# Performance work log

Hardware: AMD Instinct MI355X
Metric: run time of the kernel (lower is better)

The kernel has to match this reference:

```python
import jax, jax.numpy as jnp
import numpy as np

N = 50000
E = 1600000
F_IN = 256
HEADS = 4
HID = 32
C = 16
NEG_SLOPE = 0.2


def _add_self_loops(edge_index, n):
    loop = jnp.arange(n, dtype=edge_index.dtype)
    return jnp.concatenate([edge_index, jnp.stack([loop, loop])], axis=1)


def gat_conv(x, edge_index, W, att_src, att_dst, bias, heads, n):
    # PyG GATConv (concat=True, add_self_loops=True, inference: no dropout)
    ei = _add_self_loops(edge_index, n)
    src, dst = ei[0], ei[1]
    d = W.shape[1] // heads
    xw = (x @ W).reshape(n, heads, d)                      # [N,H,D]
    a_src = jnp.sum(xw * att_src, axis=-1)                 # [N,H]
    a_dst = jnp.sum(xw * att_dst, axis=-1)                 # [N,H]
    e = jax.nn.leaky_relu(a_src[src] + a_dst[dst], NEG_SLOPE)  # [E',H]
    # segment softmax over destination neighborhoods
    m = jax.ops.segment_max(e, dst, num_segments=n)        # [N,H]
    ex = jnp.exp(e - m[dst])
    denom = jax.ops.segment_sum(ex, dst, num_segments=n)   # [N,H]
    alpha = ex / denom[dst]                                # [E',H]
    msg = xw[src] * alpha[:, :, None]                      # [E',H,D]
    out = jax.ops.segment_sum(msg, dst, num_segments=n)    # [N,H,D]
    return out.reshape(n, heads * d) + bias


def setup_inputs() -> dict:
    key = jax.random.key(0)
    ks = jax.random.split(key, 10)
    g = lambda k, shape, fan: jax.random.normal(k, shape, jnp.float32) * (1.0 / np.sqrt(fan))
    x = jax.random.normal(ks[0], (N, F_IN), jnp.float32)
    edge_index = jax.random.randint(ks[1], (2, E), 0, N, dtype=jnp.int64)
    return {
        "x": x,
        "edge_index": edge_index,
        "W1": g(ks[2], (F_IN, HEADS * HID), F_IN),
        "att_src1": g(ks[3], (HEADS, HID), HID),
        "att_dst1": g(ks[4], (HEADS, HID), HID),
        "b1": jnp.zeros((HEADS * HID,), jnp.float32),
        "W2": g(ks[5], (HEADS * HID, C), HEADS * HID),
        "att_src2": g(ks[6], (1, C), C),
        "att_dst2": g(ks[7], (1, C), C),
        "b2": jnp.zeros((C,), jnp.float32),
    }


def reference(x, edge_index, W1, att_src1, att_dst1, b1, W2, att_src2, att_dst2, b2):
    h = gat_conv(x, edge_index, W1, att_src1, att_dst1, b1, HEADS, N)
    h = jax.nn.relu(h)
    # dropout: identity at inference (training=False)
    out = gat_conv(h, edge_index, W2, att_src2, att_dst2, b2, 1, N)
    return jax.nn.log_softmax(out, axis=1)
```

## Files before the change

### kernel.cpp

```cpp
#include <hip/hip_runtime.h>
#include <hip/hip_bf16.h>

typedef __hip_bfloat16 bf16;
typedef long long i64;
typedef unsigned long long u64;
typedef __attribute__((ext_vector_type(8))) short short8;
typedef __attribute__((ext_vector_type(4))) float floatx4;

#define NN    50000
#define EE    1600000
#define E2    1650000
#define FIN   256
#define HD    128
#define NH    4
#define NC    16
#define SLOPE 0.2f
#define K     128
#define DPB   391
#define CAPB  16384
#define CAP   15360
#define CH2   2048

#define KS_S  2312

#define OF_FLAGS 0
#define OF_BCUR  16
#define OF_BBASE 144
#define OF_RP    280
#define OF_W1T   50284
#define OF_BIN   66668
#define OF_CSR   4260972
#define OF_XQ    5910972
#define OF_SC    7510972
#define OF_AS1   7610972
#define OF_AD1   7810972
#define OF_HW2   8010972
#define OF_AS2   8810972
#define OF_AD2   8860972

__device__ __forceinline__ float b2f(bf16 v) { return __bfloat162float(v); }
__device__ __forceinline__ float us2f(unsigned short u) {
    return __uint_as_float(((unsigned)u) << 16);
}
__device__ __forceinline__ unsigned short f2us(float f) {
    unsigned u = __float_as_uint(f);
    return (unsigned short)((u + 0x7fffu + ((u >> 16) & 1u)) >> 16);
}
__device__ __forceinline__ float lrelu(float v) { return v > 0.f ? v : SLOPE * v; }
__device__ __forceinline__ float sb2f(unsigned u, int sh) {
    return (float)((int)(u << (24 - sh)) >> 24);
}
__device__ __forceinline__ int fwi(int node, int ch) {
    return node * 132 + (ch >> 5) * 33 + (ch & 31);
}

template <bool F32>
__device__ __forceinline__ float ldin(const void* p, int i) {
    if (F32) return ((const float*)p)[i];
    return b2f(((const bf16*)p)[i]);
}
template <bool F32>
__device__ __forceinline__ float4 ldin4(const void* p, int i) {
    if (F32) return *(const float4*)((const float*)p + i);
    ushort4 u = *(const ushort4*)((const unsigned short*)p + i);
    float4 r;
    r.x = us2f(u.x); r.y = us2f(u.y); r.z = us2f(u.z); r.w = us2f(u.w);
    return r;
}

__device__ __forceinline__ void edge_sd(const void* ei, int f64, int e, int& s, int& d) {
    if (e >= EE) { s = e - EE; d = s; return; }
    if (f64) {
        s = (int)((const i64*)ei)[e];
        d = (int)((const i64*)ei)[EE + e];
    } else {
        s = ((const int*)ei)[e];
        d = ((const int*)ei)[EE + e];
    }
    s = min(max(s, 0), NN - 1);
    d = min(max(d, 0), NN - 1);
}

__global__ void detect(const void* x, const void* ei, int* flags, int* bcur) {
    __shared__ int cnt[2];
    int t = threadIdx.x;
    if (t < K) bcur[t] = t * CAPB;
    if (t == 0) { cnt[0] = 0; cnt[1] = 0; }
    __syncthreads();
    const unsigned short* xb = (const unsigned short*)x;
    int c0 = 0;
    for (int i = t; i < 4096; i += 256) {
        float v = __uint_as_float(((unsigned)xb[2 * i]) << 16);
        if (!(fabsf(v) < 1e6f)) c0++;
    }
    const i64* e64 = (const i64*)ei;
    int c1 = 0;
    for (int i = t; i < 1024; i += 256) {
        i64 v = e64[i];
        if (v >= 0 && v < NN) c1++;
    }
    atomicAdd(&cnt[0], c0);
    atomicAdd(&cnt[1], c1);
    __syncthreads();
    if (t == 0) {
        flags[0] = (cnt[0] > 400) ? 1 : 0;
        flags[1] = (cnt[1] >= 1000) ? 1 : 0;
    }
}

template <bool F32>
__global__ void trW(const void* __restrict__ W1, const int* __restrict__ flags,
                    unsigned short* __restrict__ w1t) {
    if (flags[0] != (F32 ? 1 : 0)) return;
    int t = blockIdx.x * 256 + threadIdx.x;
    int k = t >> 5, n4 = (t & 31) * 4;
    float4 v = ldin4<F32>(W1, k * HD + n4);
    int ks = k >> 5, kk = k & 31;
    w1t[((ks * HD + n4 + 0) * 32) + kk] = f2us(v.x);
    w1t[((ks * HD + n4 + 1) * 32) + kk] = f2us(v.y);
    w1t[((ks * HD + n4 + 2) * 32) + kk] = f2us(v.z);
    w1t[((ks * HD + n4 + 3) * 32) + kk] = f2us(v.w);
}

__global__ __launch_bounds__(256) void binScatter(const void* __restrict__ ei,
                                                  const int* __restrict__ flags,
                                                  int* __restrict__ bcur,
                                                  u64* __restrict__ bin) {
    __shared__ int h[K], res[K];
    int t = threadIdx.x;
    int base = blockIdx.x * CH2 + t * 8;
    if (t < K) h[t] = 0;
    __syncthreads();
    int f64 = flags[1];
    int sv[8], dv[8], rk[8];
    int n_ = 0;
    if (!f64 && base + 8 <= EE) {
        const int* es = (const int*)ei;
        int4 a = *(const int4*)&es[base];
        int4 b = *(const int4*)&es[base + 4];
        int4 c = *(const int4*)&es[EE + base];
        int4 g = *(const int4*)&es[EE + base + 4];
        sv[0] = a.x; sv[1] = a.y; sv[2] = a.z; sv[3] = a.w;
        sv[4] = b.x; sv[5] = b.y; sv[6] = b.z; sv[7] = b.w;
        dv[0] = c.x; dv[1] = c.y; dv[2] = c.z; dv[3] = c.w;
        dv[4] = g.x; dv[5] = g.y; dv[6] = g.z; dv[7] = g.w;
#pragma unroll
        for (int i = 0; i < 8; i++) {
            sv[i] = min(max(sv[i], 0), NN - 1);
            dv[i] = min(max(dv[i], 0), NN - 1);
        }
        n_ = 8;
    } else {
        for (int i = 0; i < 8; i++) {
            int e = base + i;
            if (e < E2) {
                int s, d; edge_sd(ei, f64, e, s, d);
                sv[n_] = s; dv[n_] = d; n_++;
            }
        }
    }
#pragma unroll 8
    for (int i = 0; i < n_; i++) rk[i] = atomicAdd(&h[dv[i] / DPB], 1);
    __syncthreads();
    if (t < K) res[t] = h[t] ? atomicAdd(&bcur[t], h[t]) : 0;
    __syncthreads();
#pragma unroll 8
    for (int i = 0; i < n_; i++) {
        int b = dv[i] / DPB;
        int pos = res[b] + rk[i];
        pos = min(pos, (b + 1) * CAPB - 1);
        bin[pos] = (((u64)(unsigned)dv[i]) << 32) | (unsigned)sv[i];
    }
}

__global__ void bucketScan(const int* __restrict__ bcur, int* __restrict__ bbase) {
    __shared__ int sh[K];
    int t = threadIdx.x;
    int v = min(bcur[t] - t * CAPB, CAPB);
    sh[t] = v;
    __syncthreads();
    for (int off = 1; off < K; off <<= 1) {
        int u = (t >= off) ? sh[t - off] : 0;
        __syncthreads();
        sh[t] += u;
        __syncthreads();
    }
    bbase[t] = sh[t] - v;
    if (t == K - 1) bbase[K] = sh[K - 1];
}

__global__ __launch_bounds__(256) void csrB(const u64* __restrict__ bin,
                                            const int* __restrict__ bbase,
                                            int* __restrict__ rp, int* __restrict__ csr) {
    __shared__ int cnt[512];
    __shared__ int cur[DPB];
    __shared__ int buf[CAP];
    int b = blockIdx.x, t = threadIdx.x;
    int d0 = b * DPB;
    int nd = min(DPB, NN - d0);
    int src0 = b * CAPB;
    int base = bbase[b], size = bbase[b + 1] - base;
    cnt[t] = 0; cnt[t + 256] = 0;
    __syncthreads();
    for (int i = t; i < size; i += 256) {
        int d = (int)(bin[src0 + i] >> 32);
        atomicAdd(&cnt[d - d0], 1);
    }
    __syncthreads();
    int a0 = cnt[2 * t], a1 = cnt[2 * t + 1];
    int ps = a0 + a1;
    buf[t] = ps;
    __syncthreads();
    for (int off = 1; off < 256; off <<= 1) {
        int u = (t >= off) ? buf[t - off] : 0;
        __syncthreads();
        buf[t] += u;
        __syncthreads();
    }
    int ex = buf[t] - ps;
    __syncthreads();
    cnt[2 * t] = ex;
    cnt[2 * t + 1] = ex + a0;
    __syncthreads();
    for (int i = t; i < nd; i += 256) {
        rp[d0 + i] = base + cnt[i];
        cur[i] = cnt[i];
    }
    if (b == K - 1 && t == 0) rp[NN] = bbase[K];
    __syncthreads();
    if (size <= CAP) {
        for (int i = t; i < size; i += 256) {
            u64 p = bin[src0 + i];
            int pos = atomicAdd(&cur[(int)(p >> 32) - d0], 1);
            buf[pos] = (int)(unsigned)p;
        }
        __syncthreads();
        for (int i = t; i < size; i += 256) csr[base + i] = buf[i];
    } else {
        for (int i = t; i < size; i += 256) {
            u64 p = bin[src0 + i];
            int pos = base + atomicAdd(&cur[(int)(p >> 32) - d0], 1);
            csr[pos] = (int)(unsigned)p;
        }
    }
}

template <bool F32>
__global__ __launch_bounds__(256) void gemm1(
    const void* __restrict__ x, const unsigned short* __restrict__ w1t,
    const void* __restrict__ as1, const void* __restrict__ ad1,
    const int* __restrict__ flags, signed char* __restrict__ xq, float* __restrict__ sc2,
    float* __restrict__ asrc, float* __restrict__ adst) {
    if (flags[0] != (F32 ? 1 : 0)) return;
    __shared__ unsigned short af[8 * KS_S];
    __shared__ float scl[128];
    int t = threadIdx.x;
    int m0 = blockIdx.x * 64;
#pragma unroll
    for (int i = 0; i < 16; i++) {
        int slot = i * 256 + t;
        int mi = slot >> 6, k4 = (slot & 63) * 4;
        float4 v = make_float4(0.f, 0.f, 0.f, 0.f);
        if (m0 + mi < NN) v = ldin4<F32>(x, (m0 + mi) * FIN + k4);
        ushort4 o;
        o.x = f2us(v.x); o.y = f2us(v.y); o.z = f2us(v.z); o.w = f2us(v.w);
        *(ushort4*)&af[(k4 >> 5) * KS_S + mi * 36 + (k4 & 31)] = o;
    }
    __syncthreads();
    int w = t >> 6, lane = t & 63;
    int col = lane & 15, q = lane >> 4;
    floatx4 acc[4][2];
#pragma unroll
    for (int mt = 0; mt < 4; mt++)
#pragma unroll
        for (int u = 0; u < 2; u++) { acc[mt][u].x = 0.f; acc[mt][u].y = 0.f; acc[mt][u].z = 0.f; acc[mt][u].w = 0.f; }
#pragma unroll
    for (int ks = 0; ks < 8; ks++) {
        short8 bf0 = *(const short8*)&w1t[(ks * HD + w * 32 + col) * 32 + q * 8];
        short8 bf1 = *(const short8*)&w1t[(ks * HD + w * 32 + 16 + col) * 32 + q * 8];
#pragma unroll
        for (int mt = 0; mt < 4; mt++) {
            short8 afr = *(const short8*)&af[ks * KS_S + (mt * 16 + col) * 36 + q * 8];
            acc[mt][0] = __builtin_amdgcn_mfma_f32_16x16x32_bf16(afr, bf0, acc[mt][0], 0, 0, 0);
            acc[mt][1] = __builtin_amdgcn_mfma_f32_16x16x32_bf16(afr, bf1, acc[mt][1], 0, 0, 0);
        }
    }
    __syncthreads();
    float* fw = (float*)af;
#pragma unroll
    for (int mt = 0; mt < 4; mt++)
#pragma unroll
        for (int u = 0; u < 2; u++)
#pragma unroll
            for (int r = 0; r < 4; r++) {
                int node = mt * 16 + q * 4 + r;
                fw[fwi(node, w * 32 + u * 16 + col)] = acc[mt][u][r];
            }
    __syncthreads();
    int node = t >> 2, part = t & 3;
    {
        float amax = 0.f;
#pragma unroll
        for (int c = 0; c < 32; c++) amax = fmaxf(amax, fabsf(fw[fwi(node, part * 32 + c)]));
        amax = fmaxf(amax, __shfl_xor(amax, 1));
        if ((part & 1) == 0) {
            scl[node * 2 + (part >> 1)] = (amax > 0.f) ? 127.f / amax : 0.f;
            if (m0 + node < NN) sc2[(m0 + node) * 2 + (part >> 1)] = amax * (1.f / 127.f);
        }
    }
    __syncthreads();
    if (m0 + node < NN) {
        float inv = scl[node * 2 + (part >> 1)];
        unsigned dw[8];
#pragma unroll
        for (int g = 0; g < 8; g++) {
            unsigned pk = 0;
#pragma unroll
            for (int j = 0; j < 4; j++) {
                float v = fw[fwi(node, part * 32 + g * 4 + j)];
                int qi = (int)rintf(v * inv);
                qi = min(127, max(-127, qi));
                pk |= ((unsigned)(qi & 255)) << (8 * j);
            }
            dw[g] = pk;
        }
        *(uint4*)&xq[(m0 + node) * HD + part * 32]      = make_uint4(dw[0], dw[1], dw[2], dw[3]);
        *(uint4*)&xq[(m0 + node) * HD + part * 32 + 16] = make_uint4(dw[4], dw[5], dw[6], dw[7]);
        float s = 0.f, dd = 0.f;
#pragma unroll
        for (int c = 0; c < 32; c++) {
            float xv = fw[fwi(node, part * 32 + c)];
            s  += xv * ldin<F32>(as1, part * 32 + c);
            dd += xv * ldin<F32>(ad1, part * 32 + c);
        }
        asrc[(m0 + node) * NH + part] = s;
        adst[(m0 + node) * NH + part] = dd;
    }
}

template <bool F32>
__global__ __launch_bounds__(128) void node1(
    const int* __restrict__ rp, const int* __restrict__ cs,
    const float* __restrict__ asrc, const float* __restrict__ adst,
    const signed char* __restrict__ xq, const float* __restrict__ sc2,
    const void* __restrict__ b1, const void* __restrict__ W2,
    const void* __restrict__ as2, const void* __restrict__ ad2,
    const int* __restrict__ flags, float* __restrict__ hw2,
    float* __restrict__ asrc2, float* __restrict__ adst2) {
    if (flags[0] != (F32 ? 1 : 0)) return;
    int d = blockIdx.x, t = threadIdx.x;
    int beg = rp[d], end = rp[d + 1];
    __shared__ float sw[32][4];
    __shared__ int   ss[32];
    __shared__ float red[2][HD];
    __shared__ float wv[2][4];
    __shared__ float hs[HD];
    __shared__ float l2[32];
    int hw_ = t & 3;
    float adw = adst[d * NH + hw_];
    int cg = t & 15, eo = t >> 4, head = cg >> 2;
    float acc[8];
#pragma unroll
    for (int j = 0; j < 8; j++) acc[j] = 0.f;
    float wacc = 0.f;
    const unsigned* xqu = (const unsigned*)xq;
    for (int chb = beg; chb < end; chb += 32) {
        __syncthreads();
        int ec = chb + (t >> 2);
        float w = 0.f, wsc = 0.f;
        int s = 0;
        if (ec < end) {
            s = cs[ec];
            w = __expf(fminf(lrelu(asrc[s * NH + hw_] + adw), 80.f));
            wsc = w * sc2[s * 2 + (hw_ >> 1)];
        }
        sw[t >> 2][hw_] = wsc;
        if (hw_ == 0) ss[t >> 2] = s;
        wacc += w;
        __syncthreads();
        int m = min(32, end - chb);
        for (int e = eo; e < m; e += 8) {
            float we = sw[e][head];
            int s2 = ss[e];
            uint2 u = *(const uint2*)&xqu[s2 * 32 + cg * 2];
            acc[0] += we * sb2f(u.x, 0);
            acc[1] += we * sb2f(u.x, 8);
            acc[2] += we * sb2f(u.x, 16);
            acc[3] += we * sb2f(u.x, 24);
            acc[4] += we * sb2f(u.y, 0);
            acc[5] += we * sb2f(u.y, 8);
            acc[6] += we * sb2f(u.y, 16);
            acc[7] += we * sb2f(u.y, 24);
        }
    }
    wacc += __shfl_xor(wacc, 4);
    wacc += __shfl_xor(wacc, 8);
    wacc += __shfl_xor(wacc, 16);
    wacc += __shfl_xor(wacc, 32);
    int wid = t >> 6, lane = t & 63;
    if (lane < 4) wv[wid][lane] = wacc;
#pragma unroll
    for (int j = 0; j < 8; j++) {
        acc[j] += __shfl_xor(acc[j], 16);
        acc[j] += __shfl_xor(acc[j], 32);
    }
    if (lane < 16) {
#pragma unroll
        for (int j = 0; j < 8; j++) red[wid][lane * 8 + j] = acc[j];
    }
    __syncthreads();
    float tot = red[0][t] + red[1][t];
    float wt  = wv[0][t >> 5] + wv[1][t >> 5];
    hs[t] = fmaxf(tot / wt + ldin<F32>(b1, t), 0.f);
    __syncthreads();
    int j = t & 15, g = t >> 4;
    float p = 0.f;
#pragma unroll
    for (int k = 0; k < 16; k++) p += hs[g * 16 + k] * ldin<F32>(W2, (g * 16 + k) * NC + j);
    p += __shfl_xor(p, 16, 64);
    p += __shfl_xor(p, 32, 64);
    if ((t & 63) < 16) l2[(t >> 6) * 16 + j] = p;
    __syncthreads();
    if (t < 16) {
        float hw = l2[t] + l2[16 + t];
        hw2[d * NC + t] = hw;
        float a2s = hw * ldin<F32>(as2, t);
        float a2d = hw * ldin<F32>(ad2, t);
#pragma unroll
        for (int off = 8; off; off >>= 1) {
            a2s += __shfl_xor(a2s, off, 16);
            a2d += __shfl_xor(a2d, off, 16);
        }
        if (t == 0) { asrc2[d] = a2s; adst2[d] = a2d; }
    }
}

template <bool F32>
__global__ __launch_bounds__(64) void node2(
    const int* __restrict__ rp, const int* __restrict__ cs,
    const float* __restrict__ asrc2, const float* __restrict__ adst2,
    const float* __restrict__ hw2, const void* __restrict__ b2,
    const int* __restrict__ flags, void* __restrict__ out) {
    if (flags[0] != (F32 ? 1 : 0)) return;
    int d = blockIdx.x, t = threadIdx.x;
    int beg = rp[d], end = rp[d + 1];
    float ad = adst2[d];
    __shared__ float sw2[64];
    __shared__ int   ss2[64];
    int q = t & 3, eo = t >> 2;
    float4 acc = make_float4(0.f, 0.f, 0.f, 0.f);
    float wsum = 0.f;
    for (int chb = beg; chb < end; chb += 64) {
        __syncthreads();
        int ec = chb + t;
        float w = 0.f;
        int s = 0;
        if (ec < end) {
            s = cs[ec];
            w = __expf(fminf(lrelu(asrc2[s] + ad), 80.f));
        }
        sw2[t] = w;
        ss2[t] = s;
        __syncthreads();
        int m = min(64, end - chb);
        for (int e = eo; e < m; e += 16) {
            float we = sw2[e];
            float4 v = *(const float4*)&hw2[ss2[e] * NC + q * 4];
            acc.x += we * v.x; acc.y += we * v.y;
            acc.z += we * v.z; acc.w += we * v.w;
            wsum += we;
        }
    }
#pragma unroll
    for (int off = 4; off < 64; off <<= 1) {
        acc.x += __shfl_xor(acc.x, off);
        acc.y += __shfl_xor(acc.y, off);
        acc.z += __shfl_xor(acc.z, off);
        acc.w += __shfl_xor(acc.w, off);
        wsum  += __shfl_xor(wsum, off);
    }
    float rw = 1.f / wsum;
    float v0 = acc.x * rw + ldin<F32>(b2, q * 4 + 0);
    float v1 = acc.y * rw + ldin<F32>(b2, q * 4 + 1);
    float v2 = acc.z * rw + ldin<F32>(b2, q * 4 + 2);
    float v3 = acc.w * rw + ldin<F32>(b2, q * 4 + 3);
    float mx = fmaxf(fmaxf(v0, v1), fmaxf(v2, v3));
    mx = fmaxf(mx, __shfl_xor(mx, 1));
    mx = fmaxf(mx, __shfl_xor(mx, 2));
    float es = __expf(v0 - mx) + __expf(v1 - mx) + __expf(v2 - mx) + __expf(v3 - mx);
    es += __shfl_xor(es, 1);
    es += __shfl_xor(es, 2);
    float lse = mx + __logf(es);
    if (t < 4) {
        if (F32) {
            *(float4*)&((float*)out)[d * NC + q * 4] =
                make_float4(v0 - lse, v1 - lse, v2 - lse, v3 - lse);
        } else {
            bf16* o = (bf16*)out + d * NC + q * 4;
            o[0] = __float2bfloat16(v0 - lse); o[1] = __float2bfloat16(v1 - lse);
            o[2] = __float2bfloat16(v2 - lse); o[3] = __float2bfloat16(v3 - lse);
        }
    }
}

extern "C" void kernel_launch(void* const* d_in, const int* in_sizes, int n_in,
                              void* d_out, int out_size, void* d_ws, size_t ws_size,
                              hipStream_t stream) {
    const void* x   = d_in[0];
    const void* ei  = d_in[1];
    const void* W1  = d_in[2];
    const void* as1 = d_in[3];
    const void* ad1 = d_in[4];
    const void* b1  = d_in[5];
    const void* W2  = d_in[6];
    const void* as2 = d_in[7];
    const void* ad2 = d_in[8];
    const void* b2v = d_in[9];

    float* ws = (float*)d_ws;
    int* flags = (int*)(ws + OF_FLAGS);
    int* bcur  = (int*)(ws + OF_BCUR);
    int* bbase = (int*)(ws + OF_BBASE);
    int* rp    = (int*)(ws + OF_RP);
    unsigned short* w1t = (unsigned short*)(ws + OF_W1T);
    u64* bin   = (u64*)(ws + OF_BIN);
    int* csr   = (int*)(ws + OF_CSR);
    signed char* xq = (signed char*)(ws + OF_XQ);
    float* sc2   = ws + OF_SC;
    float* asrc1 = ws + OF_AS1;
    float* adst1 = ws + OF_AD1;
    float* hw2   = ws + OF_HW2;
    float* asrc2 = ws + OF_AS2;
    float* adst2 = ws + OF_AD2;

    detect<<<1, 256, 0, stream>>>(x, ei, flags, bcur);
    trW<true><<<32, 256, 0, stream>>>(W1, flags, w1t);
    binScatter<<<(E2 + CH2 - 1) / CH2, 256, 0, stream>>>(ei, flags, bcur, bin);
    bucketScan<<<1, K, 0, stream>>>(bcur, bbase);
    csrB<<<K, 256, 0, stream>>>(bin, bbase, rp, csr);

    const int GB = (NN + 63) / 64;
    gemm1<true><<<GB, 256, 0, stream>>>(x, w1t, as1, ad1, flags, xq, sc2, asrc1, adst1);
    node1<true><<<NN, 128, 0, stream>>>(rp, csr, asrc1, adst1, xq, sc2, b1, W2, as2, ad2,
                                        flags, hw2, asrc2, adst2);
    node2<true><<<NN, 64, 0, stream>>>(rp, csr, asrc2, adst2, hw2, b2v, flags, d_out);
}
```

Before: 291.4 us.

## Widen node1 to 256 threads, offset-encode int8, pack four nodes per node2 block

```diff
diff --git a/kernel.cpp b/kernel.cpp
--- a/kernel.cpp
+++ b/kernel.cpp
@@ -47,8 +47,8 @@
     return (unsigned short)((u + 0x7fffu + ((u >> 16) & 1u)) >> 16);
 }
 __device__ __forceinline__ float lrelu(float v) { return v > 0.f ? v : SLOPE * v; }
-__device__ __forceinline__ float sb2f(unsigned u, int sh) {
-    return (float)((int)(u << (24 - sh)) >> 24);
+__device__ __forceinline__ float ub2f(unsigned u, int sh) {
+    return (float)((u >> sh) & 0xffu);
 }
 __device__ __forceinline__ int fwi(int node, int ch) {
     return node * 132 + (ch >> 5) * 33 + (ch & 31);
@@ -320,7 +320,7 @@
                 float v = fw[fwi(node, part * 32 + g * 4 + j)];
                 int qi = (int)rintf(v * inv);
                 qi = min(127, max(-127, qi));
-                pk |= ((unsigned)(qi & 255)) << (8 * j);
+                pk |= ((unsigned)((qi + 128) & 255)) << (8 * j);
             }
             dw[g] = pk;
         }
@@ -339,7 +339,7 @@
 }
 
 template <bool F32>
-__global__ __launch_bounds__(128) void node1(
+__global__ __launch_bounds__(256) void node1(
     const int* __restrict__ rp, const int* __restrict__ cs,
     const float* __restrict__ asrc, const float* __restrict__ adst,
     const signed char* __restrict__ xq, const float* __restrict__ sc2,
@@ -350,21 +350,21 @@
     if (flags[0] != (F32 ? 1 : 0)) return;
     int d = blockIdx.x, t = threadIdx.x;
     int beg = rp[d], end = rp[d + 1];
-    __shared__ float sw[32][4];
-    __shared__ int   ss[32];
-    __shared__ float red[2][HD];
-    __shared__ float wv[2][4];
+    __shared__ float sw[64][5];
+    __shared__ int   ss[64];
+    __shared__ float red[4][HD];
+    __shared__ float wv[4][4];
     __shared__ float hs[HD];
-    __shared__ float l2[32];
+    __shared__ float l2[4][16];
     int hw_ = t & 3;
     float adw = adst[d * NH + hw_];
     int cg = t & 15, eo = t >> 4, head = cg >> 2;
     float acc[8];
 #pragma unroll
     for (int j = 0; j < 8; j++) acc[j] = 0.f;
-    float wacc = 0.f;
+    float wacc = 0.f, wss = 0.f;
     const unsigned* xqu = (const unsigned*)xq;
-    for (int chb = beg; chb < end; chb += 32) {
+    for (int chb = beg; chb < end; chb += 64) {
         __syncthreads();
         int ec = chb + (t >> 2);
         float w = 0.f, wsc = 0.f;
@@ -378,21 +378,25 @@
         if (hw_ == 0) ss[t >> 2] = s;
         wacc += w;
         __syncthreads();
-        int m = min(32, end - chb);
-        for (int e = eo; e < m; e += 8) {
+#pragma unroll
+        for (int k = 0; k < 4; k++) {
+            int e = eo + k * 16;
             float we = sw[e][head];
             int s2 = ss[e];
             uint2 u = *(const uint2*)&xqu[s2 * 32 + cg * 2];
-            acc[0] += we * sb2f(u.x, 0);
-            acc[1] += we * sb2f(u.x, 8);
-            acc[2] += we * sb2f(u.x, 16);
-            acc[3] += we * sb2f(u.x, 24);
-            acc[4] += we * sb2f(u.y, 0);
-            acc[5] += we * sb2f(u.y, 8);
-            acc[6] += we * sb2f(u.y, 16);
-            acc[7] += we * sb2f(u.y, 24);
-        }
-    }
+            acc[0] += we * ub2f(u.x, 0);
+            acc[1] += we * ub2f(u.x, 8);
+            acc[2] += we * ub2f(u.x, 16);
+            acc[3] += we * ub2f(u.x, 24);
+            acc[4] += we * ub2f(u.y, 0);
+            acc[5] += we * ub2f(u.y, 8);
+            acc[6] += we * ub2f(u.y, 16);
+            acc[7] += we * ub2f(u.y, 24);
+            wss += we;
+        }
+    }
+#pragma unroll
+    for (int j = 0; j < 8; j++) acc[j] -= 128.f * wss;
     wacc += __shfl_xor(wacc, 4);
     wacc += __shfl_xor(wacc, 8);
     wacc += __shfl_xor(wacc, 16);
@@ -409,20 +413,22 @@
         for (int j = 0; j < 8; j++) red[wid][lane * 8 + j] = acc[j];
     }
     __syncthreads();
-    float tot = red[0][t] + red[1][t];
-    float wt  = wv[0][t >> 5] + wv[1][t >> 5];
-    hs[t] = fmaxf(tot / wt + ldin<F32>(b1, t), 0.f);
+    if (t < HD) {
+        float tot = red[0][t] + red[1][t] + red[2][t] + red[3][t];
+        float wt  = wv[0][t >> 5] + wv[1][t >> 5] + wv[2][t >> 5] + wv[3][t >> 5];
+        hs[t] = fmaxf(tot / wt + ldin<F32>(b1, t), 0.f);
+    }
     __syncthreads();
     int j = t & 15, g = t >> 4;
     float p = 0.f;
 #pragma unroll
-    for (int k = 0; k < 16; k++) p += hs[g * 16 + k] * ldin<F32>(W2, (g * 16 + k) * NC + j);
-    p += __shfl_xor(p, 16, 64);
-    p += __shfl_xor(p, 32, 64);
-    if ((t & 63) < 16) l2[(t >> 6) * 16 + j] = p;
+    for (int k = 0; k < 8; k++) p += hs[g * 8 + k] * ldin<F32>(W2, (g * 8 + k) * NC + j);
+    p += __shfl_xor(p, 16);
+    p += __shfl_xor(p, 32);
+    if (lane < 16) l2[wid][j] = p;
     __syncthreads();
     if (t < 16) {
-        float hw = l2[t] + l2[16 + t];
+        float hw = l2[0][t] + l2[1][t] + l2[2][t] + l2[3][t];
         hw2[d * NC + t] = hw;
         float a2s = hw * ldin<F32>(as2, t);
         float a2d = hw * ldin<F32>(ad2, t);
@@ -436,39 +442,44 @@
 }
 
 template <bool F32>
-__global__ __launch_bounds__(64) void node2(
+__global__ __launch_bounds__(256) void node2(
     const int* __restrict__ rp, const int* __restrict__ cs,
     const float* __restrict__ asrc2, const float* __restrict__ adst2,
     const float* __restrict__ hw2, const void* __restrict__ b2,
     const int* __restrict__ flags, void* __restrict__ out) {
     if (flags[0] != (F32 ? 1 : 0)) return;
-    int d = blockIdx.x, t = threadIdx.x;
+    int t = threadIdx.x, wid = t >> 6, lane = t & 63;
+    int d = blockIdx.x * 4 + wid;
+    if (d >= NN) return;
     int beg = rp[d], end = rp[d + 1];
     float ad = adst2[d];
-    __shared__ float sw2[64];
-    __shared__ int   ss2[64];
-    int q = t & 3, eo = t >> 2;
+    int q = lane & 3, eo = lane >> 2;
     float4 acc = make_float4(0.f, 0.f, 0.f, 0.f);
-    float wsum = 0.f;
+    float wtot = 0.f;
     for (int chb = beg; chb < end; chb += 64) {
-        __syncthreads();
-        int ec = chb + t;
+        int ec = chb + lane;
         float w = 0.f;
         int s = 0;
         if (ec < end) {
             s = cs[ec];
             w = __expf(fminf(lrelu(asrc2[s] + ad), 80.f));
         }
-        sw2[t] = w;
-        ss2[t] = s;
-        __syncthreads();
-        int m = min(64, end - chb);
-        for (int e = eo; e < m; e += 16) {
-            float we = sw2[e];
-            float4 v = *(const float4*)&hw2[ss2[e] * NC + q * 4];
+        float ws = w;
+        ws += __shfl_xor(ws, 1);
+        ws += __shfl_xor(ws, 2);
+        ws += __shfl_xor(ws, 4);
+        ws += __shfl_xor(ws, 8);
+        ws += __shfl_xor(ws, 16);
+        ws += __shfl_xor(ws, 32);
+        wtot += ws;
+#pragma unroll
+        for (int k = 0; k < 4; k++) {
+            int e = eo + k * 16;
+            float we = __shfl(w, e);
+            int s2 = __shfl(s, e);
+            float4 v = *(const float4*)&hw2[s2 * NC + q * 4];
             acc.x += we * v.x; acc.y += we * v.y;
             acc.z += we * v.z; acc.w += we * v.w;
-            wsum += we;
         }
     }
 #pragma unroll
@@ -477,9 +488,8 @@
         acc.y += __shfl_xor(acc.y, off);
         acc.z += __shfl_xor(acc.z, off);
         acc.w += __shfl_xor(acc.w, off);
-        wsum  += __shfl_xor(wsum, off);
-    }
-    float rw = 1.f / wsum;
+    }
+    float rw = 1.f / wtot;
     float v0 = acc.x * rw + ldin<F32>(b2, q * 4 + 0);
     float v1 = acc.y * rw + ldin<F32>(b2, q * 4 + 1);
     float v2 = acc.z * rw + ldin<F32>(b2, q * 4 + 2);
@@ -491,7 +501,7 @@
     es += __shfl_xor(es, 1);
     es += __shfl_xor(es, 2);
     float lse = mx + __logf(es);
-    if (t < 4) {
+    if (lane < 4) {
         if (F32) {
             *(float4*)&((float*)out)[d * NC + q * 4] =
                 make_float4(v0 - lse, v1 - lse, v2 - lse, v3 - lse);
@@ -541,7 +551,8 @@
 
     const int GB = (NN + 63) / 64;
     gemm1<true><<<GB, 256, 0, stream>>>(x, w1t, as1, ad1, flags, xq, sc2, asrc1, adst1);
-    node1<true><<<NN, 128, 0, stream>>>(rp, csr, asrc1, adst1, xq, sc2, b1, W2, as2, ad2,
+    node1<true><<<NN, 256, 0, stream>>>(rp, csr, asrc1, adst1, xq, sc2, b1, W2, as2, ad2,
                                         flags, hw2, asrc2, adst2);
-    node2<true><<<NN, 64, 0, stream>>>(rp, csr, asrc2, adst2, hw2, b2v, flags, d_out);
-}
+    node2<true><<<(NN + 3) / 4, 256, 0, stream>>>(rp, csr, asrc2, adst2, hw2, b2v, flags,
+                                                  d_out);
+}
```

Measured after the change: 327.8 us. 12.5% more time.
